# Performance work log

Measured on AMD Instinct MI355X. Metric: run time of the kernel, lower is better.

Reference implementation:

```python
import jax, jax.numpy as jnp
import numpy as np

NUM_LAYERS = 3
CHANNELS = 8
IN_CHANNELS = 8
MASK_FEAT_STRIDE = 8
MASK_OUT_STRIDE = 4
SOI = np.array([64., 128., 256., 512., 1024.], dtype=np.float32)
WEIGHT_NUMS = [(IN_CHANNELS + 2) * CHANNELS, CHANNELS * CHANNELS, CHANNELS * 1]  # [80, 64, 8]
BIAS_NUMS = [CHANNELS, CHANNELS, 1]
NUM_GEN_PARAMS = sum(WEIGHT_NUMS) + sum(BIAS_NUMS)  # 169


def aligned_bilinear(x, factor):
    # Faithful to adet.utils.comm.aligned_bilinear
    if factor == 1:
        return x
    n, c, h, w = x.shape
    x = jnp.pad(x, ((0, 0), (0, 0), (0, 1), (0, 1)), mode='edge')  # replicate pad right/bottom
    oh, ow = factor * h + 1, factor * w + 1

    def interp_axis(t, out_len, axis):
        # align_corners=True from (in_len) to (out_len) with scale (in_len-1)/(out_len-1) == 1/factor
        src = jnp.arange(out_len, dtype=t.dtype) / factor
        i0 = jnp.floor(src).astype(jnp.int32)
        i1 = jnp.minimum(i0 + 1, t.shape[axis] - 1)
        wgt = src - i0.astype(t.dtype)
        a = jnp.take(t, i0, axis=axis)
        b = jnp.take(t, i1, axis=axis)
        shp = [1] * t.ndim
        shp[axis] = out_len
        wgt = wgt.reshape(shp)
        return a * (1 - wgt) + b * wgt

    x = interp_axis(x, oh, 2)
    x = interp_axis(x, ow, 3)
    pad = factor // 2
    x = jnp.pad(x, ((0, 0), (0, 0), (pad, 0), (pad, 0)), mode='edge')
    return x[:, :, :oh - 1, :ow - 1]


def setup_inputs() -> dict:
    key = jax.random.key(0)
    k1, k2, k3, k4, k5 = jax.random.split(key, 5)
    mask_feats = jax.random.normal(k1, (2, IN_CHANNELS, 128, 192), dtype=jnp.float32)
    mask_head_params = jax.random.normal(k2, (400, NUM_GEN_PARAMS), dtype=jnp.float32)
    inst_locations = jax.random.uniform(k3, (400, 2), dtype=jnp.float32) * 1024.0
    im_inds = jax.random.randint(k4, (400,), 0, 2, dtype=jnp.int32)
    fpn_levels = jax.random.randint(k5, (400,), 0, 5, dtype=jnp.int32)
    return {
        'mask_feats': mask_feats,
        'mask_head_params': mask_head_params,
        'inst_locations': inst_locations,
        'im_inds': im_inds,
        'fpn_levels': fpn_levels,
    }


def reference(mask_feats, mask_head_params, inst_locations, im_inds, fpn_levels):
    N, C, H, W = mask_feats.shape
    n_inst = mask_head_params.shape[0]
    dt = mask_feats.dtype

    # compute_locations: pixel centers at stride MASK_FEAT_STRIDE
    sx = jnp.arange(W, dtype=dt) * MASK_FEAT_STRIDE + MASK_FEAT_STRIDE // 2
    sy = jnp.arange(H, dtype=dt) * MASK_FEAT_STRIDE + MASK_FEAT_STRIDE // 2
    yy, xx = jnp.meshgrid(sy, sx, indexing='ij')
    locs = jnp.stack([xx.reshape(-1), yy.reshape(-1)], axis=1)  # [HW, 2] (x, y)

    # relative coords, normalized by size-of-interest per fpn level
    rel = inst_locations[:, None, :] - locs[None, :, :]          # [n, HW, 2]
    rel = jnp.transpose(rel, (0, 2, 1))                          # [n, 2, HW]
    soi = jnp.asarray(SOI, dtype=dt)[fpn_levels]                 # [n]
    rel = rel / soi[:, None, None]

    feats = mask_feats[im_inds].reshape(n_inst, IN_CHANNELS, H * W)
    x = jnp.concatenate([rel, feats], axis=1)                    # [n, 10, HW]

    # parse_dynamic_params: split into per-instance weights/biases
    offs = np.cumsum([0] + WEIGHT_NUMS + BIAS_NUMS)
    w0 = mask_head_params[:, offs[0]:offs[1]].reshape(n_inst, CHANNELS, IN_CHANNELS + 2)
    w1 = mask_head_params[:, offs[1]:offs[2]].reshape(n_inst, CHANNELS, CHANNELS)
    w2 = mask_head_params[:, offs[2]:offs[3]].reshape(n_inst, 1, CHANNELS)
    b0 = mask_head_params[:, offs[3]:offs[4]]                    # [n, 8]
    b1 = mask_head_params[:, offs[4]:offs[5]]                    # [n, 8]
    b2 = mask_head_params[:, offs[5]:offs[6]]                    # [n, 1]

    # grouped 1x1 convs == per-instance tiny GEMMs over pixels
    x = jax.nn.relu(jnp.einsum('noi,nip->nop', w0, x) + b0[:, :, None])
    x = jax.nn.relu(jnp.einsum('noi,nip->nop', w1, x) + b1[:, :, None])
    x = jnp.einsum('noi,nip->nop', w2, x) + b2[:, :, None]

    mask_logits = x.reshape(n_inst, 1, H, W)
    return aligned_bilinear(mask_logits, MASK_FEAT_STRIDE // MASK_OUT_STRIDE)
```

## Files before the change

### kernel.cpp

```cpp
#include <hip/hip_runtime.h>


#define HH   128
#define WW   192
#define OHH  256
#define OWW  384
#define THY  32
#define TWX  128
#define LR   18
#define LC   66
#define NPX  (LR*LC)
#define NPARAMS 169

__global__ __launch_bounds__(256, 2)
void dmh_fused(const float* __restrict__ mask_feats,
               const float* __restrict__ params,
               const float* __restrict__ locs,
               const int*   __restrict__ im_inds,
               const int*   __restrict__ fpn,
               float* __restrict__ out)
{
    __shared__ float sp[NPARAMS];
    __shared__ float L[LR][LC];

    const int inst = blockIdx.z;
    const int tid  = threadIdx.x;

    if (tid < NPARAMS) sp[tid] = params[(size_t)inst * NPARAMS + tid];

    const int   im     = im_inds[inst];
    const float instx  = locs[2*inst];
    const float insty  = locs[2*inst + 1];
    const float invsoi = 1.0f / (float)(64 << fpn[inst]);

    const int oy0 = blockIdx.y * THY;
    const int ox0 = blockIdx.x * TWX;
    const int r0  = oy0 >> 1;
    const int c0  = ox0 >> 1;

    __syncthreads();

    const float* __restrict__ fbase = mask_feats + (size_t)im * 8 * HH * WW;

    float xf[5][8];
    float xr[5][2];
    int   pix[5];
#pragma unroll
    for (int k = 0; k < 5; ++k) {
        int p = tid + 256*k;
        if (p > NPX-1) p = NPX-1;
        pix[k] = p;
        int lr = p / LC;
        int lc = p - lr*LC;
        int gy = r0 - 1 + lr; gy = gy < 0 ? 0 : (gy > HH-1 ? HH-1 : gy);
        int gx = c0 - 1 + lc; gx = gx < 0 ? 0 : (gx > WW-1 ? WW-1 : gx);
        xr[k][0] = (instx - (float)(gx*8 + 4)) * invsoi;
        xr[k][1] = (insty - (float)(gy*8 + 4)) * invsoi;
        const float* fp = fbase + gy*WW + gx;
#pragma unroll
        for (int c = 0; c < 8; ++c)
            xf[k][c] = fp[c*HH*WW];
    }

    float h0[5][8];
#pragma unroll
    for (int o = 0; o < 8; ++o) {
        const float w0 = sp[o*10 + 0];
        const float w1 = sp[o*10 + 1];
        float wc[8];
#pragma unroll
        for (int c = 0; c < 8; ++c) wc[c] = sp[o*10 + 2 + c];
        const float b = sp[152 + o];
#pragma unroll
        for (int k = 0; k < 5; ++k) {
            float a = w0*xr[k][0] + w1*xr[k][1];
#pragma unroll
            for (int c = 0; c < 8; ++c) a += wc[c]*xf[k][c];
            h0[k][o] = fmaxf(a + b, 0.0f);
        }
    }

    float h1[5][8];
#pragma unroll
    for (int o = 0; o < 8; ++o) {
        float wv[8];
#pragma unroll
        for (int i = 0; i < 8; ++i) wv[i] = sp[80 + o*8 + i];
        const float b = sp[160 + o];
#pragma unroll
        for (int k = 0; k < 5; ++k) {
            float a = wv[0]*h0[k][0];
#pragma unroll
            for (int i = 1; i < 8; ++i) a += wv[i]*h0[k][i];
            h1[k][o] = fmaxf(a + b, 0.0f);
        }
    }

    {
        float wv[8];
#pragma unroll
        for (int i = 0; i < 8; ++i) wv[i] = sp[144 + i];
        const float b = sp[168];
#pragma unroll
        for (int k = 0; k < 5; ++k) {
            float a = wv[0]*h1[k][0];
#pragma unroll
            for (int i = 1; i < 8; ++i) a += wv[i]*h1[k][i];
            ((float*)L)[pix[k]] = a + b;
        }
    }

    __syncthreads();

    float* __restrict__ obase = out + (size_t)inst * OHH * OWW;
#pragma unroll
    for (int j = 0; j < 4; ++j) {
        const int yl = (tid >> 5) + 8*j;
        const int xq = (tid & 31) * 4;
        const int y  = oy0 + yl;
        const int yy = (y > 0) ? (y - 1) : 0;
        const int iy0 = yy >> 1;
        const float fy = (yy & 1) ? 0.5f : 0.0f;
        const int ly = iy0 - r0 + 1;
        const int m  = (ox0 + xq) >> 1;
        const int lx = m - c0;
        float t[4];
#pragma unroll
        for (int i = 0; i < 4; ++i) {
            const float a  = L[ly  ][lx + i];
            const float bb = L[ly+1][lx + i];
            t[i] = a*(1.0f - fy) + bb*fy;
        }
        float4 r;
        r.x = 0.5f*t[0] + 0.5f*t[1];
        r.y = t[1];
        r.z = 0.5f*t[1] + 0.5f*t[2];
        r.w = t[2];
        *(float4*)(obase + (size_t)y*OWW + ox0 + xq) = r;
    }
}

extern "C" void kernel_launch(void* const* d_in, const int* in_sizes, int n_in,
                              void* d_out, int out_size, void* d_ws, size_t ws_size,
                              hipStream_t stream) {
    const float* mask_feats = (const float*)d_in[0];
    const float* params     = (const float*)d_in[1];
    const float* locs       = (const float*)d_in[2];
    const int*   im_inds    = (const int*)d_in[3];
    const int*   fpn        = (const int*)d_in[4];
    float*       out        = (float*)d_out;

    const int n_inst = in_sizes[1] / NPARAMS;
    dim3 grid(OWW/TWX, OHH/THY, n_inst);
    dmh_fused<<<grid, 256, 0, stream>>>(mask_feats, params, locs, im_inds, fpn, out);
}
```

Measured before the change: 202.1 us.

## Process pixels one at a time, read weights directly, raise occupancy

```diff
diff --git a/kernel.cpp b/kernel.cpp
--- a/kernel.cpp
+++ b/kernel.cpp
@@ -9,10 +9,11 @@
 #define TWX  128
 #define LR   18
 #define LC   66
+#define LCP  67
 #define NPX  (LR*LC)
 #define NPARAMS 169
 
-__global__ __launch_bounds__(256, 2)
+__global__ __launch_bounds__(256, 6)
 void dmh_fused(const float* __restrict__ mask_feats,
                const float* __restrict__ params,
                const float* __restrict__ locs,
@@ -20,13 +21,12 @@
                const int*   __restrict__ fpn,
                float* __restrict__ out)
 {
-    __shared__ float sp[NPARAMS];
-    __shared__ float L[LR][LC];
+    __shared__ float L[LR][LCP];
 
     const int inst = blockIdx.z;
     const int tid  = threadIdx.x;
 
-    if (tid < NPARAMS) sp[tid] = params[(size_t)inst * NPARAMS + tid];
+    const float* __restrict__ w = params + (size_t)inst * NPARAMS;
 
     const int   im     = im_inds[inst];
     const float instx  = locs[2*inst];
@@ -38,76 +38,46 @@
     const int r0  = oy0 >> 1;
     const int c0  = ox0 >> 1;
 
-    __syncthreads();
-
     const float* __restrict__ fbase = mask_feats + (size_t)im * 8 * HH * WW;
 
-    float xf[5][8];
-    float xr[5][2];
-    int   pix[5];
-#pragma unroll
+#pragma unroll 2
     for (int k = 0; k < 5; ++k) {
         int p = tid + 256*k;
         if (p > NPX-1) p = NPX-1;
-        pix[k] = p;
         int lr = p / LC;
         int lc = p - lr*LC;
         int gy = r0 - 1 + lr; gy = gy < 0 ? 0 : (gy > HH-1 ? HH-1 : gy);
         int gx = c0 - 1 + lc; gx = gx < 0 ? 0 : (gx > WW-1 ? WW-1 : gx);
-        xr[k][0] = (instx - (float)(gx*8 + 4)) * invsoi;
-        xr[k][1] = (insty - (float)(gy*8 + 4)) * invsoi;
+        const float rx = (instx - (float)(gx*8 + 4)) * invsoi;
+        const float ry = (insty - (float)(gy*8 + 4)) * invsoi;
         const float* fp = fbase + gy*WW + gx;
+
+        float xf[8];
 #pragma unroll
-        for (int c = 0; c < 8; ++c)
-            xf[k][c] = fp[c*HH*WW];
-    }
+        for (int c = 0; c < 8; ++c) xf[c] = fp[c*HH*WW];
 
-    float h0[5][8];
+        float h0[8];
 #pragma unroll
-    for (int o = 0; o < 8; ++o) {
-        const float w0 = sp[o*10 + 0];
-        const float w1 = sp[o*10 + 1];
-        float wc[8];
+        for (int o = 0; o < 8; ++o) {
+            float a = w[o*10]*rx + w[o*10 + 1]*ry;
 #pragma unroll
-        for (int c = 0; c < 8; ++c) wc[c] = sp[o*10 + 2 + c];
-        const float b = sp[152 + o];
+            for (int c = 0; c < 8; ++c) a += w[o*10 + 2 + c]*xf[c];
+            h0[o] = fmaxf(a + w[152 + o], 0.0f);
+        }
+
+        float h1[8];
 #pragma unroll
-        for (int k = 0; k < 5; ++k) {
-            float a = w0*xr[k][0] + w1*xr[k][1];
+        for (int o = 0; o < 8; ++o) {
+            float a = w[80 + o*8]*h0[0];
 #pragma unroll
-            for (int c = 0; c < 8; ++c) a += wc[c]*xf[k][c];
-            h0[k][o] = fmaxf(a + b, 0.0f);
+            for (int i = 1; i < 8; ++i) a += w[80 + o*8 + i]*h0[i];
+            h1[o] = fmaxf(a + w[160 + o], 0.0f);
         }
-    }
 
-    float h1[5][8];
+        float a = w[144]*h1[0];
 #pragma unroll
-    for (int o = 0; o < 8; ++o) {
-        float wv[8];
-#pragma unroll
-        for (int i = 0; i < 8; ++i) wv[i] = sp[80 + o*8 + i];
-        const float b = sp[160 + o];
-#pragma unroll
-        for (int k = 0; k < 5; ++k) {
-            float a = wv[0]*h0[k][0];
-#pragma unroll
-            for (int i = 1; i < 8; ++i) a += wv[i]*h0[k][i];
-            h1[k][o] = fmaxf(a + b, 0.0f);
-        }
-    }
-
-    {
-        float wv[8];
-#pragma unroll
-        for (int i = 0; i < 8; ++i) wv[i] = sp[144 + i];
-        const float b = sp[168];
-#pragma unroll
-        for (int k = 0; k < 5; ++k) {
-            float a = wv[0]*h1[k][0];
-#pragma unroll
-            for (int i = 1; i < 8; ++i) a += wv[i]*h1[k][i];
-            ((float*)L)[pix[k]] = a + b;
-        }
+        for (int i = 1; i < 8; ++i) a += w[144 + i]*h1[i];
+        L[lr][lc] = a + w[168];
     }
 
     __syncthreads();
@@ -121,15 +91,15 @@
         const int yy = (y > 0) ? (y - 1) : 0;
         const int iy0 = yy >> 1;
         const float fy = (yy & 1) ? 0.5f : 0.0f;
+        const float gy1 = 1.0f - fy;
         const int ly = iy0 - r0 + 1;
-        const int m  = (ox0 + xq) >> 1;
-        const int lx = m - c0;
-        float t[4];
+        const int lx = xq >> 1;
+        float t[3];
 #pragma unroll
-        for (int i = 0; i < 4; ++i) {
+        for (int i = 0; i < 3; ++i) {
             const float a  = L[ly  ][lx + i];
             const float bb = L[ly+1][lx + i];
-            t[i] = a*(1.0f - fy) + bb*fy;
+            t[i] = a*gy1 + bb*fy;
         }
         float4 r;
         r.x = 0.5f*t[0] + 0.5f*t[1];
```

Result: slower. 271.4 us (+34.3%).
